# Kernel tuning notes

Measured on AMD Instinct MI355X. Metric: run time of the kernel, lower is better.

## Reference

```python
import jax, jax.numpy as jnp
import numpy as np

B, T, D = 2048, 60, 6
H, F, O = 64, 10, 1


def setup_inputs() -> dict:
    key = jax.random.key(0)
    ks = jax.random.split(key, 16)
    w = lambda k, shape, s=0.1: jax.random.normal(k, shape, jnp.float32) * s
    return {
        "x": jax.random.normal(ks[0], (B, T, D), jnp.float32),
        "W_i": w(ks[1], (D, H)), "U_i": w(ks[2], (H, H)), "b_i": jnp.zeros((H,), jnp.float32),
        "W_ste": w(ks[3], (D, H)), "U_ste": w(ks[4], (H, H)), "b_ste": jnp.ones((H,), jnp.float32),
        "W_fre": w(ks[5], (D, F)), "U_fre": w(ks[6], (H, F)), "b_fre": jnp.ones((F,), jnp.float32),
        "W_c": w(ks[7], (D, H)), "U_c": w(ks[8], (H, H)), "b_c": jnp.zeros((H,), jnp.float32),
        "W_o": w(ks[9], (D, H)), "U_o": w(ks[10], (H, H)), "b_o": jnp.zeros((H,), jnp.float32),
        "U_a": w(ks[11], (F, 1)), "b_a": jnp.zeros((H,), jnp.float32),
        "W_p": w(ks[12], (H, O)), "b_p": jnp.zeros((O,), jnp.float32),
    }


def _hsig(v):
    # torch.nn.Hardsigmoid: relu6(x + 3) / 6
    return jnp.clip(v / 6.0 + 0.5, 0.0, 1.0)


def reference(x, W_i, U_i, b_i, W_ste, U_ste, b_ste, W_fre, U_fre, b_fre,
              W_c, U_c, b_c, W_o, U_o, b_o, U_a, b_a, W_p, b_p):
    b, t_len, _ = x.shape
    h_dim = W_i.shape[1]
    f_dim = W_fre.shape[1]
    freq = jnp.arange(f_dim, dtype=x.dtype) / f_dim  # (F,)
    ua = U_a[:, 0]  # (F,)

    def step(carry, x_t):
        h, S_re, S_im, t = carry
        i = _hsig(x_t @ W_i + b_i + h @ U_i)              # (B,H)
        ste = _hsig(x_t @ W_ste + b_ste + h @ U_ste)      # (B,H)
        fre = _hsig(x_t @ W_fre + b_fre + h @ U_fre)      # (B,F)
        f = ste[:, :, None] * fre[:, None, :]             # (B,H,F)
        c = i * jnp.tanh(x_t @ W_c + b_c + h @ U_c)       # (B,H)
        t = t + 1.0
        omega = (2.0 * jnp.pi) * t * freq                  # (F,)
        S_re = f * S_re + c[:, :, None] * jnp.cos(omega)   # (B,H,F)
        S_im = f * S_im + c[:, :, None] * jnp.sin(omega)   # (B,H,F)
        A = S_re * S_re + S_im * S_im                      # (B,H,F)
        a = jnp.tanh(jnp.einsum('bhf,f->bh', A, ua) + b_a)
        o = _hsig(x_t @ W_o + b_o + h @ U_o)
        h = o * a
        return (h, S_re, S_im, t), None

    init = (jnp.zeros((b, h_dim), x.dtype),
            jnp.zeros((b, h_dim, f_dim), x.dtype),
            jnp.zeros((b, h_dim, f_dim), x.dtype),
            jnp.asarray(0.0, x.dtype))
    (h, _, _, _), _ = jax.lax.scan(step, init, jnp.swapaxes(x, 0, 1))
    # original returns p from the last timestep only
    return h @ W_p + b_p
```

## Files before the change

kernel.cpp:

```cpp
#include <hip/hip_runtime.h>


#define BB 2048
#define TT 60
#define DD 6
#define HH 64
#define FF 10
#define NB 4

#define HS 72
#define XCS 964

typedef short bf16x8 __attribute__((ext_vector_type(8)));
typedef float f32x4  __attribute__((ext_vector_type(4)));

__device__ __forceinline__ unsigned short f2bf(float f) {
    union { float f; unsigned u; } v; v.f = f;
    unsigned r = v.u + 0x7fffu + ((v.u >> 16) & 1u);
    return (unsigned short)(r >> 16);
}
__device__ __forceinline__ float bf2f(unsigned short b) {
    union { unsigned u; float f; } v; v.u = ((unsigned)b) << 16; return v.f;
}
__device__ __forceinline__ float hsig_f(float v) {
    return __builtin_amdgcn_fmed3f(fmaf(v, 0.16666666666666666f, 0.5f), 0.0f, 1.0f);
}
__device__ __forceinline__ float tanh_f(float x) {
    float xc = fminf(fmaxf(x, -12.0f), 12.0f);
    float e  = __builtin_amdgcn_exp2f(xc * 2.8853900817779268f);
    return (e - 1.0f) * __builtin_amdgcn_rcpf(e + 1.0f);
}
__device__ __forceinline__ float uni(float v) {
    return __int_as_float(__builtin_amdgcn_readfirstlane(__float_as_int(v)));
}
__device__ __forceinline__ void pinv(bf16x8& v) { asm volatile("" : "+v"(v)); }

__global__ __launch_bounds__(256, 2)
void sfm_kernel(
    const float* __restrict__ x,
    const float* __restrict__ W_i,  const float* __restrict__ U_i,  const float* __restrict__ b_i,
    const float* __restrict__ W_ste,const float* __restrict__ U_ste,const float* __restrict__ b_ste,
    const float* __restrict__ W_fre,const float* __restrict__ U_fre,const float* __restrict__ b_fre,
    const float* __restrict__ W_c,  const float* __restrict__ U_c,  const float* __restrict__ b_c,
    const float* __restrict__ W_o,  const float* __restrict__ U_o,  const float* __restrict__ b_o,
    const float* __restrict__ U_a,  const float* __restrict__ b_a,
    const float* __restrict__ W_p,  const float* __restrict__ b_p,
    float* __restrict__ out)
{
    const int tid  = threadIdx.x;
    const int lane = tid & 63;
    const int wave = tid >> 6;
    const int q    = lane >> 4;
    const int n16  = lane & 15;
    const int b0   = blockIdx.x * NB;

    __shared__ __align__(16) float xc[NB * XCS];
    __shared__ __align__(16) unsigned short hhi[NB * HS];
    __shared__ __align__(16) unsigned short hlo[NB * HS];
    __shared__ __align__(16) float zbuf[4 * 64 * NB];
    __shared__ __align__(16) float frebuf[NB * 12];
    __shared__ __align__(16) float ctab[10 * 10 * 2];
    __shared__ float cstabB[10 * 2];
    __shared__ float red[4][NB];

    for (int i = tid; i < NB * TT * DD; i += 256) {
        const int b = i / (TT * DD), rem = i - b * (TT * DD);
        const int s = rem / DD, d = rem - s * DD;
        xc[b * XCS + s * 16 + d] = x[(size_t)b0 * (TT * DD) + i];
    }
    if (tid < 10) {
        const float CTc[10] = { 1.0f,  0.8090169943749475f,  0.30901699437494745f,
                               -0.30901699437494745f, -0.8090169943749475f, -1.0f,
                               -0.8090169943749475f, -0.30901699437494745f,
                                0.30901699437494745f,  0.8090169943749475f };
        const float STc[10] = { 0.0f,  0.5877852522924731f,  0.9510565162951535f,
                                0.9510565162951535f,  0.5877852522924731f,  0.0f,
                               -0.5877852522924731f, -0.9510565162951535f,
                               -0.9510565162951535f, -0.5877852522924731f };
        float cc = 0.0f, ss = 0.0f;
        #pragma unroll
        for (int j = 0; j < 10; ++j) if (tid == j) { cc = CTc[j]; ss = STc[j]; }
        cstabB[tid * 2] = cc; cstabB[tid * 2 + 1] = ss;
    }
    for (int i = tid; i < NB * HS; i += 256) { hhi[i] = 0; hlo[i] = 0; }
    __syncthreads();

    if (tid < NB * TT) {
        const int b = tid / TT, s = tid - b * TT;
        float xr[DD];
        #pragma unroll
        for (int d = 0; d < DD; ++d) xr[d] = xc[b * XCS + s * 16 + d];
        #pragma unroll
        for (int f = 0; f < FF; ++f) {
            float v = b_fre[f];
            #pragma unroll
            for (int d = 0; d < DD; ++d) v = fmaf(xr[d], W_fre[d * FF + f], v);
            xc[b * XCS + s * 16 + 6 + f] = v;
        }
    }
    if (tid < 100) {
        const int mm = tid / 10, ff = tid - mm * 10;
        const int idx = (ff * mm) % 10;
        ctab[tid * 2]     = cstabB[idx * 2];
        ctab[tid * 2 + 1] = cstabB[idx * 2 + 1];
    }

    const int NT = (wave == 0) ? 5 : 4;
    bf16x8 Bh[5][2], Bl[5][2];
    #pragma unroll
    for (int t = 0; t < 5; ++t) {
        if (t >= NT) continue;
        const bool isfre = (t == 3 && wave == 3);
        const int g  = (t == 4) ? 3 : wave;
        const int cb = (t == 3 || t == 4) ? 48 : t * 16;
        const float* Up = isfre ? U_fre :
                          (g == 0) ? U_i : (g == 1) ? U_ste : (g == 2) ? U_c : U_o;
        #pragma unroll
        for (int c = 0; c < 2; ++c) {
            #pragma unroll
            for (int j = 0; j < 8; ++j) {
                const int kv = c * 32 + q * 8 + j;
                float v;
                if (isfre) v = (n16 < FF) ? Up[kv * FF + n16] : 0.0f;
                else       v = Up[kv * HH + cb + n16];
                const unsigned short hb = f2bf(v);
                Bh[t][c][j] = (short)hb;
                Bl[t][c][j] = (short)f2bf(v - bf2f(hb));
            }
            pinv(Bh[t][c]); pinv(Bl[t][c]);
        }
    }

    const int pb = tid & (NB - 1);
    const int pc = tid >> 2;
    const float bav = b_a[pc];
    const float wpv = W_p[pc];
    const float bpv = uni(b_p[0]);
    float uav[FF];
    #pragma unroll
    for (int f = 0; f < FF; ++f) uav[f] = uni(U_a[f]);
    float wxi[DD], wxs[DD], wxc[DD], wxo[DD];
    #pragma unroll
    for (int d = 0; d < DD; ++d) {
        wxi[d] = W_i[d * HH + pc];  wxs[d] = W_ste[d * HH + pc];
        wxc[d] = W_c[d * HH + pc];  wxo[d] = W_o[d * HH + pc];
    }
    const float bi = b_i[pc], bs = b_ste[pc], bc = b_c[pc], bo = b_o[pc];

    float Sre[FF], Sim[FF];
    #pragma unroll
    for (int f = 0; f < FF; ++f) { Sre[f] = 0.0f; Sim[f] = 0.0f; }
    float hv = 0.0f;

    const int ab = n16 & (NB - 1);
    const unsigned short* hhp = &hhi[ab * HS];
    const unsigned short* hlp = &hlo[ab * HS];

    __syncthreads();

    int m = 1;
    for (int s = 0; s < TT; ++s) {
        bf16x8 Ah[2], Al[2];
        #pragma unroll
        for (int c = 0; c < 2; ++c) {
            Ah[c] = *(const bf16x8*)&hhp[c * 32 + q * 8];
            Al[c] = *(const bf16x8*)&hlp[c * 32 + q * 8];
        }

        f32x4 acc[5];
        #pragma unroll
        for (int t = 0; t < 5; ++t) {
            if (t >= NT) continue;
            f32x4 a = {0.0f, 0.0f, 0.0f, 0.0f};
            #pragma unroll
            for (int c = 0; c < 2; ++c) {
                a = __builtin_amdgcn_mfma_f32_16x16x32_bf16(Al[c], Bh[t][c], a, 0, 0, 0);
                a = __builtin_amdgcn_mfma_f32_16x16x32_bf16(Ah[c], Bl[t][c], a, 0, 0, 0);
                a = __builtin_amdgcn_mfma_f32_16x16x32_bf16(Ah[c], Bh[t][c], a, 0, 0, 0);
            }
            acc[t] = a;
        }

        if (q == 0) {
            *(f32x4*)&zbuf[(wave * 64 +  0 + n16) * NB] = acc[0];
            *(f32x4*)&zbuf[(wave * 64 + 16 + n16) * NB] = acc[1];
            *(f32x4*)&zbuf[(wave * 64 + 32 + n16) * NB] = acc[2];
            if (wave == 3) {
                if (n16 < FF) {
                    #pragma unroll
                    for (int r = 0; r < 4; ++r)
                        frebuf[r * 12 + n16] = acc[3][r] + xc[r * XCS + s * 16 + 6 + n16];
                }
            } else {
                *(f32x4*)&zbuf[(wave * 64 + 48 + n16) * NB] = acc[3];
            }
            if (wave == 0)
                *(f32x4*)&zbuf[(3 * 64 + 48 + n16) * NB] = acc[4];
        }
        __syncthreads();

        const float4 xv4 = *(const float4*)&xc[pb * XCS + s * 16];
        const float2 xv2 = *(const float2*)&xc[pb * XCS + s * 16 + 4];
        const float xa[DD] = {xv4.x, xv4.y, xv4.z, xv4.w, xv2.x, xv2.y};

        float vi = bi, vs = bs, vc = bc, vo = bo;
        #pragma unroll
        for (int d = 0; d < DD; ++d) {
            vi = fmaf(xa[d], wxi[d], vi);
            vs = fmaf(xa[d], wxs[d], vs);
            vc = fmaf(xa[d], wxc[d], vc);
            vo = fmaf(xa[d], wxo[d], vo);
        }
        const float zi = zbuf[(0 * 64 + pc) * NB + pb] + vi;
        const float zs = zbuf[(1 * 64 + pc) * NB + pb] + vs;
        const float zc = zbuf[(2 * 64 + pc) * NB + pb] + vc;
        const float zo = zbuf[(3 * 64 + pc) * NB + pb] + vo;

        const f32x4 fb0 = *(const f32x4*)&frebuf[pb * 12];
        const f32x4 fb1 = *(const f32x4*)&frebuf[pb * 12 + 4];
        const f32x4 fb2 = *(const f32x4*)&frebuf[pb * 12 + 8];
        float fr[FF];
        #pragma unroll
        for (int f = 0; f < 4; ++f) fr[f] = hsig_f(fb0[f]);
        #pragma unroll
        for (int f = 0; f < 4; ++f) fr[4 + f] = hsig_f(fb1[f]);
        fr[8] = hsig_f(fb2[0]); fr[9] = hsig_f(fb2[1]);

        const float iv  = hsig_f(zi);
        const float stv = hsig_f(zs);
        const float ov  = hsig_f(zo);
        const float cv  = iv * tanh_f(zc);

        const float* tp = &ctab[m * 20];
        float aacc = bav;
        #pragma unroll
        for (int f = 0; f < FF; ++f) {
            const float2 tv = *(const float2*)&tp[f * 2];
            const float fc = stv * fr[f];
            Sre[f] = fmaf(fc, Sre[f], cv * tv.x);
            Sim[f] = fmaf(fc, Sim[f], cv * tv.y);
            const float A = fmaf(Sim[f], Sim[f], Sre[f] * Sre[f]);
            aacc = fmaf(A, uav[f], aacc);
        }
        hv = ov * tanh_f(aacc);

        {
            const unsigned short hb = f2bf(hv);
            hhi[pb * HS + pc] = hb;
            hlo[pb * HS + pc] = f2bf(hv - bf2f(hb));
        }
        if (++m == 10) m = 0;
        __syncthreads();
    }

    float val = hv * wpv;
    val += __shfl_xor(val, 4, 64);
    val += __shfl_xor(val, 8, 64);
    val += __shfl_xor(val, 16, 64);
    val += __shfl_xor(val, 32, 64);
    if (lane < NB) red[wave][lane] = val;
    __syncthreads();
    if (tid < NB)
        out[b0 + tid] = red[0][tid] + red[1][tid] + red[2][tid] + red[3][tid] + bpv;
}

extern "C" void kernel_launch(void* const* d_in, const int* in_sizes, int n_in,
                              void* d_out, int out_size, void* d_ws, size_t ws_size,
                              hipStream_t stream) {
    (void)in_sizes; (void)n_in; (void)d_ws; (void)ws_size; (void)out_size;
    const float* x     = (const float*)d_in[0];
    const float* W_i   = (const float*)d_in[1];
    const float* U_i   = (const float*)d_in[2];
    const float* b_i   = (const float*)d_in[3];
    const float* W_ste = (const float*)d_in[4];
    const float* U_ste = (const float*)d_in[5];
    const float* b_ste = (const float*)d_in[6];
    const float* W_fre = (const float*)d_in[7];
    const float* U_fre = (const float*)d_in[8];
    const float* b_fre = (const float*)d_in[9];
    const float* W_c   = (const float*)d_in[10];
    const float* U_c   = (const float*)d_in[11];
    const float* b_c   = (const float*)d_in[12];
    const float* W_o   = (const float*)d_in[13];
    const float* U_o   = (const float*)d_in[14];
    const float* b_o   = (const float*)d_in[15];
    const float* U_a   = (const float*)d_in[16];
    const float* b_a   = (const float*)d_in[17];
    const float* W_p   = (const float*)d_in[18];
    const float* b_p   = (const float*)d_in[19];

    sfm_kernel<<<BB / NB, 256, 0, stream>>>(
        x, W_i, U_i, b_i, W_ste, U_ste, b_ste, W_fre, U_fre, b_fre,
        W_c, U_c, b_c, W_o, U_o, b_o, U_a, b_a, W_p, b_p, (float*)d_out);
}
```

Measured before the change: 159.1 us.

## Interleave two batch groups per block to overlap MFMA and pointwise phases

```diff
diff --git a/kernel.cpp b/kernel.cpp
--- a/kernel.cpp
+++ b/kernel.cpp
@@ -6,7 +6,7 @@
 #define DD 6
 #define HH 64
 #define FF 10
-#define NB 4
+#define NB 8
 
 #define HS 72
 #define XCS 964
@@ -35,7 +35,8 @@
 }
 __device__ __forceinline__ void pinv(bf16x8& v) { asm volatile("" : "+v"(v)); }
 
-__global__ __launch_bounds__(256, 2)
+__global__ __launch_bounds__(256)
+__attribute__((amdgpu_waves_per_eu(1, 1)))
 void sfm_kernel(
     const float* __restrict__ x,
     const float* __restrict__ W_i,  const float* __restrict__ U_i,  const float* __restrict__ b_i,
@@ -57,8 +58,10 @@
     __shared__ __align__(16) float xc[NB * XCS];
     __shared__ __align__(16) unsigned short hhi[NB * HS];
     __shared__ __align__(16) unsigned short hlo[NB * HS];
-    __shared__ __align__(16) float zbuf[4 * 64 * NB];
-    __shared__ __align__(16) float frebuf[NB * 12];
+    __shared__ __align__(16) float zbA[4 * 64 * 4];
+    __shared__ __align__(16) float zbB[4 * 64 * 4];
+    __shared__ __align__(16) float fbA[4 * 12];
+    __shared__ __align__(16) float fbB[4 * 12];
     __shared__ __align__(16) float ctab[10 * 10 * 2];
     __shared__ float cstabB[10 * 2];
     __shared__ float red[4][NB];
@@ -85,8 +88,8 @@
     for (int i = tid; i < NB * HS; i += 256) { hhi[i] = 0; hlo[i] = 0; }
     __syncthreads();
 
-    if (tid < NB * TT) {
-        const int b = tid / TT, s = tid - b * TT;
+    for (int item = tid; item < NB * TT; item += 256) {
+        const int b = item / TT, s = item - b * TT;
         float xr[DD];
         #pragma unroll
         for (int d = 0; d < DD; ++d) xr[d] = xc[b * XCS + s * 16 + d];
@@ -131,7 +134,7 @@
         }
     }
 
-    const int pb = tid & (NB - 1);
+    const int pb = tid & 3;
     const int pc = tid >> 2;
     const float bav = b_a[pc];
     const float wpv = W_p[pc];
@@ -147,26 +150,24 @@
     }
     const float bi = b_i[pc], bs = b_ste[pc], bc = b_c[pc], bo = b_o[pc];
 
-    float Sre[FF], Sim[FF];
+    float Sre[2][FF], Sim[2][FF], hv[2];
     #pragma unroll
-    for (int f = 0; f < FF; ++f) { Sre[f] = 0.0f; Sim[f] = 0.0f; }
-    float hv = 0.0f;
-
-    const int ab = n16 & (NB - 1);
-    const unsigned short* hhp = &hhi[ab * HS];
-    const unsigned short* hlp = &hlo[ab * HS];
-
-    __syncthreads();
-
-    int m = 1;
-    for (int s = 0; s < TT; ++s) {
+    for (int f = 0; f < FF; ++f) {
+        Sre[0][f] = 0.0f; Sim[0][f] = 0.0f;
+        Sre[1][f] = 0.0f; Sim[1][f] = 0.0f;
+    }
+    hv[0] = 0.0f; hv[1] = 0.0f;
+
+    auto do_M = [&](const int g, const int s, float* zb, float* fb) {
+        const int ab = g * 4 + (n16 & 3);
+        const unsigned short* hhp = &hhi[ab * HS];
+        const unsigned short* hlp = &hlo[ab * HS];
         bf16x8 Ah[2], Al[2];
         #pragma unroll
         for (int c = 0; c < 2; ++c) {
             Ah[c] = *(const bf16x8*)&hhp[c * 32 + q * 8];
             Al[c] = *(const bf16x8*)&hlp[c * 32 + q * 8];
         }
-
         f32x4 acc[5];
         #pragma unroll
         for (int t = 0; t < 5; ++t) {
@@ -180,27 +181,29 @@
             }
             acc[t] = a;
         }
-
         if (q == 0) {
-            *(f32x4*)&zbuf[(wave * 64 +  0 + n16) * NB] = acc[0];
-            *(f32x4*)&zbuf[(wave * 64 + 16 + n16) * NB] = acc[1];
-            *(f32x4*)&zbuf[(wave * 64 + 32 + n16) * NB] = acc[2];
+            *(f32x4*)&zb[(wave * 64 +  0 + n16) * 4] = acc[0];
+            *(f32x4*)&zb[(wave * 64 + 16 + n16) * 4] = acc[1];
+            *(f32x4*)&zb[(wave * 64 + 32 + n16) * 4] = acc[2];
             if (wave == 3) {
                 if (n16 < FF) {
                     #pragma unroll
                     for (int r = 0; r < 4; ++r)
-                        frebuf[r * 12 + n16] = acc[3][r] + xc[r * XCS + s * 16 + 6 + n16];
+                        fb[r * 12 + n16] = acc[3][r] + xc[(g * 4 + r) * XCS + s * 16 + 6 + n16];
                 }
             } else {
-                *(f32x4*)&zbuf[(wave * 64 + 48 + n16) * NB] = acc[3];
+                *(f32x4*)&zb[(wave * 64 + 48 + n16) * 4] = acc[3];
             }
             if (wave == 0)
-                *(f32x4*)&zbuf[(3 * 64 + 48 + n16) * NB] = acc[4];
-        }
-        __syncthreads();
-
-        const float4 xv4 = *(const float4*)&xc[pb * XCS + s * 16];
-        const float2 xv2 = *(const float2*)&xc[pb * XCS + s * 16 + 4];
+                *(f32x4*)&zb[(3 * 64 + 48 + n16) * 4] = acc[4];
+        }
+    };
+
+    auto do_P = [&](const int g, const int s, const float* zb, const float* fb,
+                    const float* tp) {
+        const int pbg = g * 4 + pb;
+        const float4 xv4 = *(const float4*)&xc[pbg * XCS + s * 16];
+        const float2 xv2 = *(const float2*)&xc[pbg * XCS + s * 16 + 4];
         const float xa[DD] = {xv4.x, xv4.y, xv4.z, xv4.w, xv2.x, xv2.y};
 
         float vi = bi, vs = bs, vc = bc, vo = bo;
@@ -211,14 +214,14 @@
             vc = fmaf(xa[d], wxc[d], vc);
             vo = fmaf(xa[d], wxo[d], vo);
         }
-        const float zi = zbuf[(0 * 64 + pc) * NB + pb] + vi;
-        const float zs = zbuf[(1 * 64 + pc) * NB + pb] + vs;
-        const float zc = zbuf[(2 * 64 + pc) * NB + pb] + vc;
-        const float zo = zbuf[(3 * 64 + pc) * NB + pb] + vo;
-
-        const f32x4 fb0 = *(const f32x4*)&frebuf[pb * 12];
-        const f32x4 fb1 = *(const f32x4*)&frebuf[pb * 12 + 4];
-        const f32x4 fb2 = *(const f32x4*)&frebuf[pb * 12 + 8];
+        const float zi = zb[(0 * 64 + pc) * 4 + pb] + vi;
+        const float zs = zb[(1 * 64 + pc) * 4 + pb] + vs;
+        const float zc = zb[(2 * 64 + pc) * 4 + pb] + vc;
+        const float zo = zb[(3 * 64 + pc) * 4 + pb] + vo;
+
+        const f32x4 fb0 = *(const f32x4*)&fb[pb * 12];
+        const f32x4 fb1 = *(const f32x4*)&fb[pb * 12 + 4];
+        const f32x4 fb2 = *(const f32x4*)&fb[pb * 12 + 8];
         float fr[FF];
         #pragma unroll
         for (int f = 0; f < 4; ++f) fr[f] = hsig_f(fb0[f]);
@@ -231,34 +234,51 @@
         const float ov  = hsig_f(zo);
         const float cv  = iv * tanh_f(zc);
 
-        const float* tp = &ctab[m * 20];
         float aacc = bav;
         #pragma unroll
         for (int f = 0; f < FF; ++f) {
             const float2 tv = *(const float2*)&tp[f * 2];
             const float fc = stv * fr[f];
-            Sre[f] = fmaf(fc, Sre[f], cv * tv.x);
-            Sim[f] = fmaf(fc, Sim[f], cv * tv.y);
-            const float A = fmaf(Sim[f], Sim[f], Sre[f] * Sre[f]);
+            Sre[g][f] = fmaf(fc, Sre[g][f], cv * tv.x);
+            Sim[g][f] = fmaf(fc, Sim[g][f], cv * tv.y);
+            const float A = fmaf(Sim[g][f], Sim[g][f], Sre[g][f] * Sre[g][f]);
             aacc = fmaf(A, uav[f], aacc);
         }
-        hv = ov * tanh_f(aacc);
-
-        {
-            const unsigned short hb = f2bf(hv);
-            hhi[pb * HS + pc] = hb;
-            hlo[pb * HS + pc] = f2bf(hv - bf2f(hb));
-        }
+        hv[g] = ov * tanh_f(aacc);
+
+        const unsigned short hb = f2bf(hv[g]);
+        hhi[pbg * HS + pc] = hb;
+        hlo[pbg * HS + pc] = f2bf(hv[g] - bf2f(hb));
+    };
+
+    __syncthreads();
+
+    do_M(0, 0, zbA, fbA);
+    __syncthreads();
+
+    int m = 1;
+    for (int s = 0; s < TT; ++s) {
+        const float* tp = &ctab[m * 20];
+        do_M(1, s, zbB, fbB);
+        do_P(0, s, zbA, fbA, tp);
+        __syncthreads();
+        if (s + 1 < TT) do_M(0, s + 1, zbA, fbA);
+        do_P(1, s, zbB, fbB, tp);
+        __syncthreads();
         if (++m == 10) m = 0;
-        __syncthreads();
-    }
-
-    float val = hv * wpv;
-    val += __shfl_xor(val, 4, 64);
-    val += __shfl_xor(val, 8, 64);
-    val += __shfl_xor(val, 16, 64);
-    val += __shfl_xor(val, 32, 64);
-    if (lane < NB) red[wave][lane] = val;
+    }
+
+    float v0 = hv[0] * wpv;
+    v0 += __shfl_xor(v0, 4, 64);
+    v0 += __shfl_xor(v0, 8, 64);
+    v0 += __shfl_xor(v0, 16, 64);
+    v0 += __shfl_xor(v0, 32, 64);
+    float v1 = hv[1] * wpv;
+    v1 += __shfl_xor(v1, 4, 64);
+    v1 += __shfl_xor(v1, 8, 64);
+    v1 += __shfl_xor(v1, 16, 64);
+    v1 += __shfl_xor(v1, 32, 64);
+    if (lane < 4) { red[wave][lane] = v0; red[wave][4 + lane] = v1; }
     __syncthreads();
     if (tid < NB)
         out[b0 + tid] = red[0][tid] + red[1][tid] + red[2][tid] + red[3][tid] + bpv;
```

After: 191.1 us. +20.1%, slower.

## Pack h hi/lo split into MFMA rows to cut MFMA count per step

Applied to the files above, without the earlier changes.

```diff
diff --git a/kernel.cpp b/kernel.cpp
--- a/kernel.cpp
+++ b/kernel.cpp
@@ -10,6 +10,7 @@
 
 #define HS 72
 #define XCS 964
+#define ZOFF 1024
 
 typedef short bf16x8 __attribute__((ext_vector_type(8)));
 typedef float f32x4  __attribute__((ext_vector_type(4)));
@@ -55,10 +56,9 @@
     const int b0   = blockIdx.x * NB;
 
     __shared__ __align__(16) float xc[NB * XCS];
-    __shared__ __align__(16) unsigned short hhi[NB * HS];
-    __shared__ __align__(16) unsigned short hlo[NB * HS];
-    __shared__ __align__(16) float zbuf[4 * 64 * NB];
-    __shared__ __align__(16) float frebuf[NB * 12];
+    __shared__ __align__(16) unsigned short hsp[16 * HS];
+    __shared__ __align__(16) float zb2[2 * 4 * 64 * 4];
+    __shared__ __align__(16) float fb[NB * 12];
     __shared__ __align__(16) float ctab[10 * 10 * 2];
     __shared__ float cstabB[10 * 2];
     __shared__ float red[4][NB];
@@ -82,7 +82,7 @@
         for (int j = 0; j < 10; ++j) if (tid == j) { cc = CTc[j]; ss = STc[j]; }
         cstabB[tid * 2] = cc; cstabB[tid * 2 + 1] = ss;
     }
-    for (int i = tid; i < NB * HS; i += 256) { hhi[i] = 0; hlo[i] = 0; }
+    for (int i = tid; i < 16 * HS; i += 256) hsp[i] = 0;
     __syncthreads();
 
     if (tid < NB * TT) {
@@ -152,50 +152,46 @@
     for (int f = 0; f < FF; ++f) { Sre[f] = 0.0f; Sim[f] = 0.0f; }
     float hv = 0.0f;
 
-    const int ab = n16 & (NB - 1);
-    const unsigned short* hhp = &hhi[ab * HS];
-    const unsigned short* hlp = &hlo[ab * HS];
+    const unsigned short* hrp = &hsp[n16 * HS];
 
     __syncthreads();
 
     int m = 1;
     for (int s = 0; s < TT; ++s) {
-        bf16x8 Ah[2], Al[2];
-        #pragma unroll
-        for (int c = 0; c < 2; ++c) {
-            Ah[c] = *(const bf16x8*)&hhp[c * 32 + q * 8];
-            Al[c] = *(const bf16x8*)&hlp[c * 32 + q * 8];
-        }
+        bf16x8 A0 = *(const bf16x8*)&hrp[0 * 32 + q * 8];
+        bf16x8 A1 = *(const bf16x8*)&hrp[1 * 32 + q * 8];
 
         f32x4 acc[5];
         #pragma unroll
         for (int t = 0; t < 5; ++t) {
             if (t >= NT) continue;
             f32x4 a = {0.0f, 0.0f, 0.0f, 0.0f};
+            a = __builtin_amdgcn_mfma_f32_16x16x32_bf16(A0, Bh[t][0], a, 0, 0, 0);
+            a = __builtin_amdgcn_mfma_f32_16x16x32_bf16(A0, Bl[t][0], a, 0, 0, 0);
+            a = __builtin_amdgcn_mfma_f32_16x16x32_bf16(A1, Bh[t][1], a, 0, 0, 0);
+            a = __builtin_amdgcn_mfma_f32_16x16x32_bf16(A1, Bl[t][1], a, 0, 0, 0);
+            acc[t] = a;
+        }
+
+        if (q < 2) {
+            float* zq = &zb2[q * ZOFF];
+            *(f32x4*)&zq[(wave * 64 +  0 + n16) * 4] = acc[0];
+            *(f32x4*)&zq[(wave * 64 + 16 + n16) * 4] = acc[1];
+            *(f32x4*)&zq[(wave * 64 + 32 + n16) * 4] = acc[2];
+            if (wave != 3)
+                *(f32x4*)&zq[(wave * 64 + 48 + n16) * 4] = acc[3];
+            if (wave == 0)
+                *(f32x4*)&zq[(3 * 64 + 48 + n16) * 4] = acc[4];
+        }
+        if (wave == 3) {
+            f32x4 af = acc[3];
             #pragma unroll
-            for (int c = 0; c < 2; ++c) {
-                a = __builtin_amdgcn_mfma_f32_16x16x32_bf16(Al[c], Bh[t][c], a, 0, 0, 0);
-                a = __builtin_amdgcn_mfma_f32_16x16x32_bf16(Ah[c], Bl[t][c], a, 0, 0, 0);
-                a = __builtin_amdgcn_mfma_f32_16x16x32_bf16(Ah[c], Bh[t][c], a, 0, 0, 0);
+            for (int r = 0; r < 4; ++r) af[r] += __shfl_xor(acc[3][r], 16, 64);
+            if (q == 0 && n16 < FF) {
+                #pragma unroll
+                for (int r = 0; r < 4; ++r)
+                    fb[r * 12 + n16] = af[r] + xc[r * XCS + s * 16 + 6 + n16];
             }
-            acc[t] = a;
-        }
-
-        if (q == 0) {
-            *(f32x4*)&zbuf[(wave * 64 +  0 + n16) * NB] = acc[0];
-            *(f32x4*)&zbuf[(wave * 64 + 16 + n16) * NB] = acc[1];
-            *(f32x4*)&zbuf[(wave * 64 + 32 + n16) * NB] = acc[2];
-            if (wave == 3) {
-                if (n16 < FF) {
-                    #pragma unroll
-                    for (int r = 0; r < 4; ++r)
-                        frebuf[r * 12 + n16] = acc[3][r] + xc[r * XCS + s * 16 + 6 + n16];
-                }
-            } else {
-                *(f32x4*)&zbuf[(wave * 64 + 48 + n16) * NB] = acc[3];
-            }
-            if (wave == 0)
-                *(f32x4*)&zbuf[(3 * 64 + 48 + n16) * NB] = acc[4];
         }
         __syncthreads();
 
@@ -211,14 +207,15 @@
             vc = fmaf(xa[d], wxc[d], vc);
             vo = fmaf(xa[d], wxo[d], vo);
         }
-        const float zi = zbuf[(0 * 64 + pc) * NB + pb] + vi;
-        const float zs = zbuf[(1 * 64 + pc) * NB + pb] + vs;
-        const float zc = zbuf[(2 * 64 + pc) * NB + pb] + vc;
-        const float zo = zbuf[(3 * 64 + pc) * NB + pb] + vo;
-
-        const f32x4 fb0 = *(const f32x4*)&frebuf[pb * 12];
-        const f32x4 fb1 = *(const f32x4*)&frebuf[pb * 12 + 4];
-        const f32x4 fb2 = *(const f32x4*)&frebuf[pb * 12 + 8];
+        const int zo4 = pc * 4 + pb;
+        const float zi = zb2[(0 * 64) * 4 + zo4] + zb2[ZOFF + (0 * 64) * 4 + zo4] + vi;
+        const float zs = zb2[(1 * 64) * 4 + zo4] + zb2[ZOFF + (1 * 64) * 4 + zo4] + vs;
+        const float zc = zb2[(2 * 64) * 4 + zo4] + zb2[ZOFF + (2 * 64) * 4 + zo4] + vc;
+        const float zo = zb2[(3 * 64) * 4 + zo4] + zb2[ZOFF + (3 * 64) * 4 + zo4] + vo;
+
+        const f32x4 fb0 = *(const f32x4*)&fb[pb * 12];
+        const f32x4 fb1 = *(const f32x4*)&fb[pb * 12 + 4];
+        const f32x4 fb2 = *(const f32x4*)&fb[pb * 12 + 8];
         float fr[FF];
         #pragma unroll
         for (int f = 0; f < 4; ++f) fr[f] = hsig_f(fb0[f]);
@@ -232,7 +229,7 @@
         const float cv  = iv * tanh_f(zc);
 
         const float* tp = &ctab[m * 20];
-        float aacc = bav;
+        float aacc0 = bav, aacc1 = 0.0f;
         #pragma unroll
         for (int f = 0; f < FF; ++f) {
             const float2 tv = *(const float2*)&tp[f * 2];
@@ -240,14 +237,15 @@
             Sre[f] = fmaf(fc, Sre[f], cv * tv.x);
             Sim[f] = fmaf(fc, Sim[f], cv * tv.y);
             const float A = fmaf(Sim[f], Sim[f], Sre[f] * Sre[f]);
-            aacc = fmaf(A, uav[f], aacc);
-        }
-        hv = ov * tanh_f(aacc);
+            if (f & 1) aacc1 = fmaf(A, uav[f], aacc1);
+            else       aacc0 = fmaf(A, uav[f], aacc0);
+        }
+        hv = ov * tanh_f(aacc0 + aacc1);
 
         {
             const unsigned short hb = f2bf(hv);
-            hhi[pb * HS + pc] = hb;
-            hlo[pb * HS + pc] = f2bf(hv - bf2f(hb));
+            hsp[pb * HS + pc]       = hb;
+            hsp[(4 + pb) * HS + pc] = f2bf(hv - bf2f(hb));
         }
         if (++m == 10) m = 0;
         __syncthreads();
```

Result: slower. 163.4 us (+2.7%).
